# Optimization experiments

Measured on AMD Instinct MI355X. Metric: run time of the kernel, lower is better.

## Reference

```python
import jax, jax.numpy as jnp
import numpy as np

N_HEAD = 16  # from init_kwargs

def setup_inputs() -> dict:
    key = jax.random.key(0)
    k1, k2, k3 = jax.random.split(key, 3)
    B, T, C = 2, 2048, 1024
    x = jax.random.normal(k1, (B, T, C), dtype=jnp.float32)
    W_qkv = jax.random.normal(k2, (3 * C, C), dtype=jnp.float32) * (1.0 / np.sqrt(C))
    W_proj = jax.random.normal(k3, (C, C), dtype=jnp.float32) * (1.0 / np.sqrt(C))
    b_proj = jnp.zeros((C,), dtype=jnp.float32)
    return {"x": x, "W_qkv": W_qkv, "W_proj": W_proj, "b_proj": b_proj}

def reference(x, W_qkv, W_proj, b_proj):
    B, T, C = x.shape
    H = N_HEAD
    hs = C // H
    # QKV projection (bias=False), split heads
    qkv = (x @ W_qkv.T).reshape(B, T, 3, H, hs)
    q = jnp.transpose(qkv[:, :, 0], (0, 2, 1, 3))  # [B,H,T,hs]
    k = jnp.transpose(qkv[:, :, 1], (0, 2, 1, 3))
    v = jnp.transpose(qkv[:, :, 2], (0, 2, 1, 3))
    scale = np.float32(1.0 / np.sqrt(hs))
    s = jnp.einsum('bhqd,bhkd->bhqk', q, k) * scale  # [B,H,T,T]
    # sp2norm: softplus weights, causal-masked, normalized by row L2 norm
    w = jax.nn.softplus(s)
    causal = jnp.tril(jnp.ones((T, T), dtype=bool))
    w = jnp.where(causal[None, None], w, jnp.float32(0.0))
    norm = jnp.sqrt(jnp.sum(w * w, axis=-1, keepdims=True))  # [B,H,T,1]
    out = jnp.einsum('bhqk,bhkd->bhqd', w, v) / norm  # [B,H,T,hs]
    out = jnp.transpose(out, (0, 2, 1, 3)).reshape(B, T, C)
    return out @ W_proj.T + b_proj
```

## Files before the change

### kernel.cpp

```cpp
#include <hip/hip_runtime.h>
#include <cstdint>
#include <cstddef>

typedef __bf16 bf16_t;
typedef __bf16 bf16x8 __attribute__((ext_vector_type(8)));
typedef __bf16 bf16x4 __attribute__((ext_vector_type(4)));
typedef float  f32x4  __attribute__((ext_vector_type(4)));
typedef unsigned int u32x2 __attribute__((ext_vector_type(2)));
typedef unsigned int u32x4 __attribute__((ext_vector_type(4)));

#define MFMA_BF16(a, b, c) __builtin_amdgcn_mfma_f32_16x16x32_bf16((a), (b), (c), 0, 0, 0)

__device__ __forceinline__ void async_load16(const void* g, void* l) {
    __builtin_amdgcn_global_load_lds((const __attribute__((address_space(1))) void*)g,
                                     (__attribute__((address_space(3))) void*)l,
                                     16, 0, 0);
}

#define SWZ(r, cg) ((((r) << 3) | ((cg) ^ ((r) & 7))) << 3)

#define Bq   2
#define Tq   2048
#define Cq   1024
#define Hq   16
#define HSq  64
#define Mrows 4096

#define QSCALE 0.18033688f

__global__ __launch_bounds__(256)
void cvt_all(const float* __restrict__ x, const float* __restrict__ wqkv,
             const float* __restrict__ wproj,
             bf16_t* __restrict__ xb, bf16_t* __restrict__ wqkvb,
             bf16_t* __restrict__ wprojb) {
    size_t gid = (size_t)blockIdx.x * 256 + threadIdx.x;
    const float* src; bf16_t* dst; size_t off;
    if (gid < 1048576)      { src = x;     dst = xb;     off = gid; }
    else if (gid < 1835008) { src = wqkv;  dst = wqkvb;  off = gid - 1048576; }
    else                    { src = wproj; dst = wprojb; off = gid - 1835008; }
    float4 v = ((const float4*)src)[off];
    bf16x4 o;
    o[0] = (bf16_t)v.x; o[1] = (bf16_t)v.y; o[2] = (bf16_t)v.z; o[3] = (bf16_t)v.w;
    *(bf16x4*)(dst + off * 4) = o;
}

template <int BM, int EPI>
__global__ __launch_bounds__(256)
void gemm_bt(const bf16_t* __restrict__ A, const bf16_t* __restrict__ B,
             void* __restrict__ Cout, const float* __restrict__ bias,
             bf16_t* __restrict__ qc, bf16_t* __restrict__ kc, bf16_t* __restrict__ vtp,
             int M, int N, int K) {
    constexpr int MR = BM / 32;
    constexpr int ACH = BM * 8 / 256;
    __shared__ __align__(16) bf16_t As[BM * 64];
    __shared__ __align__(16) bf16_t Bs[128 * 64];

    const int tid  = threadIdx.x;
    const int wave = tid >> 6;
    const int lane = tid & 63;
    const int m0 = blockIdx.y * BM;
    const int n0 = blockIdx.x * 128;
    const int wm = (wave >> 1) * (BM / 2);
    const int wn = (wave & 1) * 64;
    const int lrow = lane & 15;
    const int lg   = lane >> 4;

    f32x4 acc[MR][4] = {};

    const bf16_t* Ag = A + (size_t)m0 * K;
    const bf16_t* Bg = B + (size_t)n0 * K;

    for (int k0 = 0; k0 < K; k0 += 64) {
        #pragma unroll
        for (int i = 0; i < ACH; i++) {
            int s = i * 256 + tid;
            int r = s >> 3, cg = (s & 7) ^ (r & 7);
            async_load16(Ag + (size_t)r * K + k0 + cg * 8, &As[s * 8]);
        }
        #pragma unroll
        for (int i = 0; i < 4; i++) {
            int s = i * 256 + tid;
            int r = s >> 3, cg = (s & 7) ^ (r & 7);
            async_load16(Bg + (size_t)r * K + k0 + cg * 8, &Bs[s * 8]);
        }
        __syncthreads();

        #pragma unroll
        for (int kk = 0; kk < 2; kk++) {
            bf16x8 af[MR], bfr[4];
            #pragma unroll
            for (int r = 0; r < MR; r++)
                af[r] = *(const bf16x8*)&As[SWZ(wm + r * 16 + lrow, kk * 4 + lg)];
            #pragma unroll
            for (int c = 0; c < 4; c++)
                bfr[c] = *(const bf16x8*)&Bs[SWZ(wn + c * 16 + lrow, kk * 4 + lg)];
            #pragma unroll
            for (int r = 0; r < MR; r++)
                #pragma unroll
                for (int c = 0; c < 4; c++)
                    acc[r][c] = MFMA_BF16(af[r], bfr[c], acc[r][c]);
        }
        __syncthreads();
    }

    const int er = (lane >> 4) * 4;
    const int ec = lane & 15;
    #pragma unroll
    for (int r = 0; r < MR; r++) {
        #pragma unroll
        for (int c = 0; c < 4; c++) {
            int m = m0 + wm + r * 16 + er;
            int n = n0 + wn + c * 16 + ec;
            if (EPI == 1) {
                #pragma unroll
                for (int v = 0; v < 4; v++)
                    ((float*)Cout)[(size_t)(m + v) * N + n] = acc[r][c][v] + bias[n];
            } else {
                int bb = m >> 11, t = m & 2047;
                if (n < 1024) {
                    #pragma unroll
                    for (int v = 0; v < 4; v++)
                        qc[(size_t)(m + v) * 1024 + n] = (bf16_t)(acc[r][c][v] * QSCALE);
                } else if (n < 2048) {
                    int h = (n - 1024) >> 6, d = (n - 1024) & 63;
                    bf16_t* p = kc + ((size_t)(bb * 16 + h) * Tq + t) * 64 + d;
                    #pragma unroll
                    for (int v = 0; v < 4; v++) p[v * 64] = (bf16_t)acc[r][c][v];
                } else {
                    int h = (n - 2048) >> 6, d = (n - 2048) & 63;
                    bf16x4 o;
                    #pragma unroll
                    for (int v = 0; v < 4; v++) o[v] = (bf16_t)acc[r][c][v];
                    *(bf16x4*)&vtp[((size_t)(bb * 16 + h) * 64 + d) * Tq + t] = o;
                }
            }
        }
    }
}

__global__ __launch_bounds__(256)
void attn_kernel(const bf16_t* __restrict__ Qc, const bf16_t* __restrict__ Kc,
                 const bf16_t* __restrict__ Vt,
                 bf16_t* __restrict__ Op0, bf16_t* __restrict__ Op1,
                 float* __restrict__ n2part) {
    __shared__ __align__(16) bf16_t Ks[2][64 * 64];
    __shared__ __align__(16) bf16_t Vs[2][64 * 64];

    const int tid = threadIdx.x;
    const int wave = tid >> 6;
    const int lane = tid & 63;
    const int lrow = lane & 15;
    const int lg   = lane >> 4;
    const int er = lg * 4;
    const int ec = lane & 15;

    const int raw  = blockIdx.y;
    const int qi   = 31 - (raw >> 1);
    const int half = raw & 1;
    const int q0   = qi * 64;
    const int bh = blockIdx.x;
    const int b = bh >> 4, h = bh & 15;

    const int nt = qi + 1;
    const int lo = (half * nt) >> 1;
    const int hi = ((half + 1) * nt) >> 1;

    const bf16_t* Qb = Qc + (size_t)b * Tq * Cq + h * 64;
    const bf16_t* Kb = Kc + (size_t)bh * Tq * 64;
    const bf16_t* Vb = Vt + (size_t)bh * 64 * Tq;

    bf16x8 qf[2];
    {
        const bf16_t* qrow = Qb + (size_t)(q0 + wave * 16 + lrow) * Cq + lg * 8;
        qf[0] = *(const bf16x8*)(qrow);
        qf[1] = *(const bf16x8*)(qrow + 32);
    }

    const int s0 = tid, s1 = tid + 256;
    const int r0 = s0 >> 3, cg0 = (s0 & 7) ^ (r0 & 7);
    const int r1 = s1 >> 3, cg1 = (s1 & 7) ^ (r1 & 7);

    bf16x8 kr0, kr1, vr0, vr1;
    if (lo < hi) {
        const int key0 = lo * 64;
        kr0 = *(const bf16x8*)&Kb[(size_t)(key0 + r0) * 64 + cg0 * 8];
        kr1 = *(const bf16x8*)&Kb[(size_t)(key0 + r1) * 64 + cg1 * 8];
        vr0 = *(const bf16x8*)&Vb[(size_t)r0 * Tq + key0 + cg0 * 8];
        vr1 = *(const bf16x8*)&Vb[(size_t)r1 * Tq + key0 + cg1 * 8];
    }

    f32x4 oacc[4] = {};
    float n2a = 0.f, n2b = 0.f;
    int cur = 0;

    for (int kt = lo; kt < hi; kt++) {
        bf16_t* ksp = Ks[cur];
        bf16_t* vsp = Vs[cur];
        *(bf16x8*)&ksp[s0 * 8] = kr0;
        *(bf16x8*)&ksp[s1 * 8] = kr1;
        *(bf16x8*)&vsp[s0 * 8] = vr0;
        *(bf16x8*)&vsp[s1 * 8] = vr1;

        if (kt + 1 < hi) {
            const int k1 = (kt + 1) * 64;
            kr0 = *(const bf16x8*)&Kb[(size_t)(k1 + r0) * 64 + cg0 * 8];
            kr1 = *(const bf16x8*)&Kb[(size_t)(k1 + r1) * 64 + cg1 * 8];
            vr0 = *(const bf16x8*)&Vb[(size_t)r0 * Tq + k1 + cg0 * 8];
            vr1 = *(const bf16x8*)&Vb[(size_t)r1 * Tq + k1 + cg1 * 8];
        }

        __syncthreads();

        f32x4 sacc[4];
        #pragma unroll
        for (int j = 0; j < 4; j++) {
            int r = j * 16 + lrow;
            bf16x8 kf0 = *(const bf16x8*)&ksp[SWZ(r, lg)];
            bf16x8 kf1 = *(const bf16x8*)&ksp[SWZ(r, 4 + lg)];
            f32x4 z = {};
            z = MFMA_BF16(kf0, qf[0], z);
            sacc[j] = MFMA_BF16(kf1, qf[1], z);
        }

        const bool diag = (kt == qi);
        uint32_t pk[4][2];
        #pragma unroll
        for (int j = 0; j < 4; j++) {
            bf16x4 wb;
            #pragma unroll
            for (int v = 0; v < 4; v++) {
                float u = __builtin_amdgcn_exp2f(sacc[j][v]);
                float w = __builtin_amdgcn_logf(1.f + u);
                if (diag && (j * 16 + er + v > wave * 16 + ec)) w = 0.f;
                if (j & 1) n2b += w * w; else n2a += w * w;
                wb[v] = (bf16_t)w;
            }
            u32x2 pw = *(u32x2*)&wb;
            pk[j][0] = pw.x; pk[j][1] = pw.y;
        }

        #pragma unroll
        for (int s2 = 0; s2 < 2; s2++) {
            u32x2 t0 = __builtin_amdgcn_permlane32_swap(pk[2 * s2][0], pk[2 * s2 + 1][0],
                                                        false, false);
            u32x2 w02 = __builtin_amdgcn_permlane16_swap(t0.x, t0.y, false, false);
            u32x2 t1 = __builtin_amdgcn_permlane32_swap(pk[2 * s2][1], pk[2 * s2 + 1][1],
                                                        false, false);
            u32x2 w13 = __builtin_amdgcn_permlane16_swap(t1.x, t1.y, false, false);
            u32x4 ww = {w02.x, w13.x, w02.y, w13.y};
            bf16x8 wf = *(bf16x8*)&ww;
            #pragma unroll
            for (int jd = 0; jd < 4; jd++) {
                bf16x8 vf = *(const bf16x8*)&vsp[SWZ(jd * 16 + lrow, s2 * 4 + lg)];
                oacc[jd] = MFMA_BF16(wf, vf, oacc[jd]);
            }
        }
        cur ^= 1;
    }

    float n2 = n2a + n2b;
    n2 += __shfl_xor(n2, 16, 64);
    n2 += __shfl_xor(n2, 32, 64);

    bf16_t* Op = (half == 0 ? Op0 : Op1) + ((size_t)bh * 32 + qi) * 4096;
    #pragma unroll
    for (int jd = 0; jd < 4; jd++) {
        #pragma unroll
        for (int v = 0; v < 4; v++) {
            Op[(wave * 16 + er + v) * 64 + jd * 16 + ec] = (bf16_t)oacc[jd][v];
        }
    }
    if (lg == 0) {
        n2part[((size_t)half * 1024 + bh * 32 + qi) * 64 + wave * 16 + ec] = n2;
    }
}

__global__ __launch_bounds__(256)
void combine_kernel(const bf16_t* __restrict__ O0, const bf16_t* __restrict__ O1,
                    const float* __restrict__ n2part, bf16_t* __restrict__ ao) {
    const int qi = blockIdx.x;
    const int bh = blockIdx.y;
    const int b = bh >> 4, h = bh & 15;
    const int t = threadIdx.x;
    const size_t base = ((size_t)bh * 32 + qi) * 4096;
    const float* np = n2part + ((size_t)bh * 32 + qi) * 64;
    #pragma unroll
    for (int i = 0; i < 2; i++) {
        int idx = i * 2048 + t * 8;
        int row = idx >> 6, col = idx & 63;
        bf16x8 a0 = *(const bf16x8*)(O0 + base + idx);
        bf16x8 a1 = *(const bf16x8*)(O1 + base + idx);
        float nsum = np[row] + np[(size_t)1024 * 64 + row];
        float inv = rsqrtf(nsum);
        bf16x8 o;
        #pragma unroll
        for (int j = 0; j < 8; j++)
            o[j] = (bf16_t)(((float)a0[j] + (float)a1[j]) * inv);
        *(bf16x8*)(ao + (size_t)(b * Tq + qi * 64 + row) * Cq + h * HSq + col) = o;
    }
}

extern "C" void kernel_launch(void* const* d_in, const int* in_sizes, int n_in,
                              void* d_out, int out_size, void* d_ws, size_t ws_size,
                              hipStream_t stream) {
    const float* x     = (const float*)d_in[0];
    const float* wqkv  = (const float*)d_in[1];
    const float* wproj = (const float*)d_in[2];
    const float* bproj = (const float*)d_in[3];
    float* out = (float*)d_out;

    char* ws = (char*)d_ws;
    bf16_t* wprojb = (bf16_t*)(ws);
    bf16_t* xb     = (bf16_t*)(ws + ( 2u << 20));
    bf16_t* wqkvb  = (bf16_t*)(ws + (10u << 20));
    bf16_t* qcb    = (bf16_t*)(ws + (16u << 20));
    bf16_t* kcb    = (bf16_t*)(ws + (24u << 20));
    bf16_t* vtb    = (bf16_t*)(ws + (32u << 20));
    bf16_t* opart0 = (bf16_t*)(ws + ( 2u << 20));
    float*  n2part = (float*)(ws + (10u << 20));
    bf16_t* opart1 = (bf16_t*)(ws + (40u << 20));
    bf16_t* aob    = (bf16_t*)(ws + (24u << 20));

    cvt_all<<<8192, 256, 0, stream>>>(x, wqkv, wproj, xb, wqkvb, wprojb);

    gemm_bt<128, 2><<<dim3(24, 32), 256, 0, stream>>>(xb, wqkvb, nullptr, nullptr,
                                                      qcb, kcb, vtb, Mrows, 3 * Cq, Cq);
    attn_kernel<<<dim3(32, 64), 256, 0, stream>>>(qcb, kcb, vtb,
                                                  opart0, opart1, n2part);
    combine_kernel<<<dim3(32, 32), 256, 0, stream>>>(opart0, opart1, n2part, aob);
    gemm_bt<64, 1><<<dim3(8, 64), 256, 0, stream>>>(aob, wprojb, (void*)out, bproj,
                                                    nullptr, nullptr, nullptr, Mrows, Cq, Cq);
}
```

Measured before the change: 172.9 us.

## Drop split-KV attention and fuse norm combine into attention epilogue

Each attention block now processes the full causal key range for its query tile, instead of two blocks each taking half and writing partial outputs. The L2-norm reciprocal is applied in the epilogue via a lane shuffle, and the result is written straight into the projection input buffer. This removes the combine kernel launch and the round trip of the partial outputs and norms through global memory. The cost is half as many blocks and a longer critical path for the last query tiles, which may worsen load balance across CUs.

```diff
diff --git a/kernel.cpp b/kernel.cpp
--- a/kernel.cpp
+++ b/kernel.cpp
@@ -140,9 +140,7 @@
 
 __global__ __launch_bounds__(256)
 void attn_kernel(const bf16_t* __restrict__ Qc, const bf16_t* __restrict__ Kc,
-                 const bf16_t* __restrict__ Vt,
-                 bf16_t* __restrict__ Op0, bf16_t* __restrict__ Op1,
-                 float* __restrict__ n2part) {
+                 const bf16_t* __restrict__ Vt, bf16_t* __restrict__ ao) {
     __shared__ __align__(16) bf16_t Ks[2][64 * 64];
     __shared__ __align__(16) bf16_t Vs[2][64 * 64];
 
@@ -154,16 +152,12 @@
     const int er = lg * 4;
     const int ec = lane & 15;
 
-    const int raw  = blockIdx.y;
-    const int qi   = 31 - (raw >> 1);
-    const int half = raw & 1;
-    const int q0   = qi * 64;
+    const int qi = 31 - blockIdx.y;
+    const int q0 = qi * 64;
     const int bh = blockIdx.x;
     const int b = bh >> 4, h = bh & 15;
 
-    const int nt = qi + 1;
-    const int lo = (half * nt) >> 1;
-    const int hi = ((half + 1) * nt) >> 1;
+    const int hi = qi + 1;
 
     const bf16_t* Qb = Qc + (size_t)b * Tq * Cq + h * 64;
     const bf16_t* Kb = Kc + (size_t)bh * Tq * 64;
@@ -181,19 +175,18 @@
     const int r1 = s1 >> 3, cg1 = (s1 & 7) ^ (r1 & 7);
 
     bf16x8 kr0, kr1, vr0, vr1;
-    if (lo < hi) {
-        const int key0 = lo * 64;
-        kr0 = *(const bf16x8*)&Kb[(size_t)(key0 + r0) * 64 + cg0 * 8];
-        kr1 = *(const bf16x8*)&Kb[(size_t)(key0 + r1) * 64 + cg1 * 8];
-        vr0 = *(const bf16x8*)&Vb[(size_t)r0 * Tq + key0 + cg0 * 8];
-        vr1 = *(const bf16x8*)&Vb[(size_t)r1 * Tq + key0 + cg1 * 8];
+    {
+        kr0 = *(const bf16x8*)&Kb[(size_t)r0 * 64 + cg0 * 8];
+        kr1 = *(const bf16x8*)&Kb[(size_t)r1 * 64 + cg1 * 8];
+        vr0 = *(const bf16x8*)&Vb[(size_t)r0 * Tq + cg0 * 8];
+        vr1 = *(const bf16x8*)&Vb[(size_t)r1 * Tq + cg1 * 8];
     }
 
     f32x4 oacc[4] = {};
     float n2a = 0.f, n2b = 0.f;
     int cur = 0;
 
-    for (int kt = lo; kt < hi; kt++) {
+    for (int kt = 0; kt < hi; kt++) {
         bf16_t* ksp = Ks[cur];
         bf16_t* vsp = Vs[cur];
         *(bf16x8*)&ksp[s0 * 8] = kr0;
@@ -262,41 +255,14 @@
     n2 += __shfl_xor(n2, 16, 64);
     n2 += __shfl_xor(n2, 32, 64);
 
-    bf16_t* Op = (half == 0 ? Op0 : Op1) + ((size_t)bh * 32 + qi) * 4096;
+    bf16_t* aop = ao + ((size_t)(b * Tq + q0 + wave * 16) * Cq) + h * HSq;
     #pragma unroll
-    for (int jd = 0; jd < 4; jd++) {
-        #pragma unroll
-        for (int v = 0; v < 4; v++) {
-            Op[(wave * 16 + er + v) * 64 + jd * 16 + ec] = (bf16_t)oacc[jd][v];
-        }
-    }
-    if (lg == 0) {
-        n2part[((size_t)half * 1024 + bh * 32 + qi) * 64 + wave * 16 + ec] = n2;
-    }
-}
-
-__global__ __launch_bounds__(256)
-void combine_kernel(const bf16_t* __restrict__ O0, const bf16_t* __restrict__ O1,
-                    const float* __restrict__ n2part, bf16_t* __restrict__ ao) {
-    const int qi = blockIdx.x;
-    const int bh = blockIdx.y;
-    const int b = bh >> 4, h = bh & 15;
-    const int t = threadIdx.x;
-    const size_t base = ((size_t)bh * 32 + qi) * 4096;
-    const float* np = n2part + ((size_t)bh * 32 + qi) * 64;
-    #pragma unroll
-    for (int i = 0; i < 2; i++) {
-        int idx = i * 2048 + t * 8;
-        int row = idx >> 6, col = idx & 63;
-        bf16x8 a0 = *(const bf16x8*)(O0 + base + idx);
-        bf16x8 a1 = *(const bf16x8*)(O1 + base + idx);
-        float nsum = np[row] + np[(size_t)1024 * 64 + row];
-        float inv = rsqrtf(nsum);
-        bf16x8 o;
-        #pragma unroll
-        for (int j = 0; j < 8; j++)
-            o[j] = (bf16_t)(((float)a0[j] + (float)a1[j]) * inv);
-        *(bf16x8*)(ao + (size_t)(b * Tq + qi * 64 + row) * Cq + h * HSq + col) = o;
+    for (int v = 0; v < 4; v++) {
+        float inv = rsqrtf(__shfl(n2, er + v, 16));
+        #pragma unroll
+        for (int jd = 0; jd < 4; jd++) {
+            aop[(size_t)(er + v) * Cq + jd * 16 + ec] = (bf16_t)(oacc[jd][v] * inv);
+        }
     }
 }
 
@@ -316,18 +282,13 @@
     bf16_t* qcb    = (bf16_t*)(ws + (16u << 20));
     bf16_t* kcb    = (bf16_t*)(ws + (24u << 20));
     bf16_t* vtb    = (bf16_t*)(ws + (32u << 20));
-    bf16_t* opart0 = (bf16_t*)(ws + ( 2u << 20));
-    float*  n2part = (float*)(ws + (10u << 20));
-    bf16_t* opart1 = (bf16_t*)(ws + (40u << 20));
-    bf16_t* aob    = (bf16_t*)(ws + (24u << 20));
+    bf16_t* aob    = (bf16_t*)(ws + ( 2u << 20));
 
     cvt_all<<<8192, 256, 0, stream>>>(x, wqkv, wproj, xb, wqkvb, wprojb);
 
     gemm_bt<128, 2><<<dim3(24, 32), 256, 0, stream>>>(xb, wqkvb, nullptr, nullptr,
                                                       qcb, kcb, vtb, Mrows, 3 * Cq, Cq);
-    attn_kernel<<<dim3(32, 64), 256, 0, stream>>>(qcb, kcb, vtb,
-                                                  opart0, opart1, n2part);
-    combine_kernel<<<dim3(32, 32), 256, 0, stream>>>(opart0, opart1, n2part, aob);
+    attn_kernel<<<dim3(32, 32), 256, 0, stream>>>(qcb, kcb, vtb, aob);
     gemm_bt<64, 1><<<dim3(8, 64), 256, 0, stream>>>(aob, wprojb, (void*)out, bproj,
                                                     nullptr, nullptr, nullptr, Mrows, Cq, Cq);
 }
```

Measured after the change: 167.8 us. 2.9% less time.
